# Kernel tuning notes

Hardware: AMD Instinct MI355X
Metric: run time of the kernel (lower is better)

Reference implementation:

```python
import jax, jax.numpy as jnp
import numpy as np

L, B, T, D, H, M = 2, 4, 1024, 256, 4, 1024
EPS = 1e-5  # hk.LayerNorm default


def setup_inputs() -> dict:
    key = jax.random.key(0)
    ks = jax.random.split(key, 12)
    s_in = (2.0 / D) ** 0.5       # VarianceScaling(2.0), fan_in = D
    s_o = (2.0 / (H * D)) ** 0.5  # fan_in = H*D for final projection
    s_m = (1.0 / M) ** 0.5
    g = lambda k, shape, s: jax.random.normal(k, shape, jnp.float32) * s
    return {
        "queries": g(ks[0], (B, T, D), 1.0),
        "Wq": g(ks[1], (L, D, H * D), s_in),
        "bq": jnp.zeros((L, H * D), jnp.float32),
        "Wk": g(ks[2], (L, D, H * D), s_in),
        "bk": jnp.zeros((L, H * D), jnp.float32),
        "Wv": g(ks[3], (L, D, H * D), s_in),
        "bv": jnp.zeros((L, H * D), jnp.float32),
        "Wo": g(ks[4], (L, H * D, D), s_o),
        "bo": jnp.zeros((L, D), jnp.float32),
        "ln1_s": jnp.ones((L, D), jnp.float32),
        "ln1_b": jnp.zeros((L, D), jnp.float32),
        "W1": g(ks[5], (L, D, M), s_in),
        "b1": jnp.zeros((L, M), jnp.float32),
        "W2": g(ks[6], (L, M, D), s_m),
        "b2": jnp.zeros((L, D), jnp.float32),
        "ln2_s": jnp.ones((L, D), jnp.float32),
        "ln2_b": jnp.zeros((L, D), jnp.float32),
    }


def _layernorm(x, s, o):
    m = jnp.mean(x, axis=-1, keepdims=True)
    v = jnp.var(x, axis=-1, keepdims=True)
    return (x - m) * jax.lax.rsqrt(v + EPS) * s + o


def _block(x, Wq, bq, Wk, bk, Wv, bv, Wo, bo, ln1_s, ln1_b, W1, b1, W2, b2, ln2_s, ln2_b):
    # Multi-head self-attention with per-head dim = D (key_size == qkv_size)
    q = (x @ Wq + bq).reshape(B, T, H, D)
    k = (x @ Wk + bk).reshape(B, T, H, D)
    v = (x @ Wv + bv).reshape(B, T, H, D)
    q = q / jnp.sqrt(jnp.float32(D))
    attn = jnp.einsum('bqhd,bkhd->bhqk', q, k)   # [B,H,T,T]
    attn = jax.nn.softmax(attn, axis=-1)
    o = jnp.einsum('bhqk,bkhd->bqhd', attn, v).reshape(B, T, H * D)
    o = o @ Wo + bo
    # post-norm residual 1
    x = _layernorm(o + x, ln1_s, ln1_b)
    # MLP: Linear(D->M) + ReLU + Linear(M->D)
    h = jax.nn.relu(x @ W1 + b1)
    m = h @ W2 + b2
    return _layernorm(m + x, ln2_s, ln2_b)


def reference(queries, Wq, bq, Wk, bk, Wv, bv, Wo, bo, ln1_s, ln1_b,
              W1, b1, W2, b2, ln2_s, ln2_b):
    x = queries
    for i in range(L):
        x = _block(x, Wq[i], bq[i], Wk[i], bk[i], Wv[i], bv[i], Wo[i], bo[i],
                   ln1_s[i], ln1_b[i], W1[i], b1[i], W2[i], b2[i],
                   ln2_s[i], ln2_b[i])
    return x
```

## Files before the change

kernel.cpp:

```cpp
#include <hip/hip_runtime.h>
#include <hip/hip_bf16.h>

#define CL 2
#define CB 4
#define CT 1024
#define CD 256
#define CH 4
#define CM 1024
#define CHD (CH * CD)
#define NROW (CB * CT)

typedef unsigned short ushort_t;
typedef __attribute__((ext_vector_type(8))) short short8v;
typedef __attribute__((ext_vector_type(4))) float float4v;
typedef __attribute__((ext_vector_type(16))) float float16v;

#define LOG2E 1.44269504088896f

__device__ __forceinline__ float bf2f(unsigned short u) {
    return __uint_as_float(((unsigned int)u) << 16);
}
__device__ __forceinline__ unsigned short f2bf(float f) {
    unsigned int x = __float_as_uint(f);
    return (unsigned short)((x + 0x7fffu + ((x >> 16) & 1u)) >> 16);
}

__global__ __launch_bounds__(256) void detect_kernel(
    const ushort_t* __restrict__ w, int n, int* __restrict__ flag)
{
    __shared__ int red[256];
    int c = 0;
    for (int i = threadIdx.x; i < n; i += 256) {
        float v = bf2f(w[i]);
        if (!(fabsf(v) <= 1e6f)) c++;
    }
    red[threadIdx.x] = c;
    __syncthreads();
    for (int s = 128; s > 0; s >>= 1) {
        if (threadIdx.x < s) red[threadIdx.x] += red[threadIdx.x + s];
        __syncthreads();
    }
    if (threadIdx.x == 0) flag[0] = (red[0] < 8) ? 1 : 0;
}

__global__ __launch_bounds__(256) void tconv_all(
    const void* __restrict__ Wq, const void* __restrict__ Wk,
    const void* __restrict__ Wv, const void* __restrict__ W1,
    ushort_t* __restrict__ wqkvT, ushort_t* __restrict__ w1T,
    const int* __restrict__ flagp)
{
    const int fbf = *flagp;
    const int z = blockIdx.z;
    const int which = z >> 1, l = z & 1;
    const void* in = (which == 0) ? Wq : (which == 1) ? Wk
                   : (which == 2) ? Wv : W1;
    ushort_t* out = (which < 3)
        ? wqkvT + (long)l * 3072 * 256 + (long)which * 1024 * 256
        : w1T + (long)l * 1024 * 256;
    const long zi = (long)l * 262144;

    __shared__ float tile[32][33];
    const int r0 = blockIdx.y * 32;
    const int c0 = blockIdx.x * 32;
    const int tx = threadIdx.x & 31;
    const int ty = threadIdx.x >> 5;
#pragma unroll
    for (int i = 0; i < 32; i += 8) {
        const long idx = zi + (long)(r0 + ty + i) * 1024 + c0 + tx;
        tile[ty + i][tx] = fbf ? bf2f(((const ushort_t*)in)[idx])
                               : ((const float*)in)[idx];
    }
    __syncthreads();
#pragma unroll
    for (int i = 0; i < 32; i += 8)
        out[(long)(c0 + ty + i) * 256 + r0 + tx] = f2bf(tile[tx][ty + i]);
}

__global__ __launch_bounds__(256) void qkv_tconv(
    const ushort_t* __restrict__ A, const ushort_t* __restrict__ B,
    const void* __restrict__ bq, const void* __restrict__ bk,
    const void* __restrict__ bv, ushort_t* __restrict__ qk,
    ushort_t* __restrict__ vT,
    const void* __restrict__ Wo, const void* __restrict__ W2,
    ushort_t* __restrict__ wscr,
    long boff, long ioff, const int* __restrict__ flagp)
{
    __shared__ __align__(16) ushort_t As[128 * 40];
    __shared__ __align__(16) ushort_t Bs[128 * 40];
    __shared__ float tile[32][33];

    const int fbf = *flagp;
    const int bx = blockIdx.x;
    const int tid = threadIdx.x;

    if (bx >= 768) {
        const int t = bx - 768;
        const int zx = t & 7;
        const int zy = (t >> 3) & 31;
        const int zz = t >> 8;
        const void* in = zz ? W2 : Wo;
        ushort_t* out = wscr + (long)zz * 262144;
        const int r0 = zy * 32;
        const int c0 = zx * 32;
        const int tx = tid & 31;
        const int ty = tid >> 5;
#pragma unroll
        for (int i = 0; i < 32; i += 8) {
            const long idx = ioff + (long)(r0 + ty + i) * 256 + c0 + tx;
            tile[ty + i][tx] = fbf ? bf2f(((const ushort_t*)in)[idx])
                                   : ((const float*)in)[idx];
        }
        __syncthreads();
#pragma unroll
        for (int i = 0; i < 32; i += 8)
            out[(long)(c0 + ty + i) * 1024 + r0 + tx] = f2bf(tile[tx][ty + i]);
        return;
    }

    const int nt = bx % 24;
    const int mt = bx / 24;
    const long m0 = (long)mt * 128;
    const long n0 = (long)nt * 128;

    const int wave = tid >> 6;
    const int lane = tid & 63;
    const int quad = lane >> 4;
    const int lrow = lane & 15;
    const int wm = (wave >> 1) * 64;
    const int wn = (wave & 1) * 64;

    float4v acc[4][4];
#pragma unroll
    for (int i = 0; i < 4; ++i)
#pragma unroll
        for (int j = 0; j < 4; ++j)
            acc[i][j] = (float4v){0.f, 0.f, 0.f, 0.f};

    for (int k0 = 0; k0 < 256; k0 += 32) {
        __syncthreads();
#pragma unroll
        for (int p = 0; p < 2; ++p) {
            const int c = p * 256 + tid;
            const int row = c >> 2;
            const int kk = (c & 3) << 3;
            *reinterpret_cast<short8v*>(&As[row * 40 + kk]) =
                *reinterpret_cast<const short8v*>(&A[(m0 + row) * 256 + k0 + kk]);
            *reinterpret_cast<short8v*>(&Bs[row * 40 + kk]) =
                *reinterpret_cast<const short8v*>(&B[(n0 + row) * 256 + k0 + kk]);
        }
        __syncthreads();

        short8v af[4], bfv[4];
#pragma unroll
        for (int i = 0; i < 4; ++i) {
            af[i]  = *reinterpret_cast<const short8v*>(&As[(wm + i * 16 + lrow) * 40 + quad * 8]);
            bfv[i] = *reinterpret_cast<const short8v*>(&Bs[(wn + i * 16 + lrow) * 40 + quad * 8]);
        }
#pragma unroll
        for (int mi = 0; mi < 4; ++mi)
#pragma unroll
            for (int ni = 0; ni < 4; ++ni)
                acc[mi][ni] = __builtin_amdgcn_mfma_f32_16x16x32_bf16(
                    af[mi], bfv[ni], acc[mi][ni], 0, 0, 0);
    }

#pragma unroll
    for (int mi = 0; mi < 4; ++mi) {
#pragma unroll
        for (int ni = 0; ni < 4; ++ni) {
            const long col = n0 + wn + ni * 16 + lrow;
            const long row0 = m0 + wm + mi * 16 + quad * 4;
            const void* bp;
            long bn;
            if (col < 1024)      { bp = bq; bn = col; }
            else if (col < 2048) { bp = bk; bn = col - 1024; }
            else                 { bp = bv; bn = col - 2048; }
            const float bias = fbf ? bf2f(((const ushort_t*)bp)[boff + bn])
                                   : ((const float*)bp)[boff + bn];
            if (col < 2048) {
#pragma unroll
                for (int r = 0; r < 4; ++r)
                    qk[(row0 + r) * 2048 + col] = f2bf(acc[mi][ni][r] + bias);
            } else {
                const long d = col - 2048;
                const long addr = ((row0 >> 10) << 2) * 262144 + d * 1024 + (row0 & 1023);
                ushort4 u;
                u.x = f2bf(acc[mi][ni][0] + bias);
                u.y = f2bf(acc[mi][ni][1] + bias);
                u.z = f2bf(acc[mi][ni][2] + bias);
                u.w = f2bf(acc[mi][ni][3] + bias);
                *reinterpret_cast<ushort4*>(&vT[addr]) = u;
            }
        }
    }
}

template <int AMODE>
__global__ __launch_bounds__(256) void mgemm64s(
    const ushort_t* __restrict__ A, const ushort_t* __restrict__ Ap1,
    const float2* __restrict__ ml, const ushort_t* __restrict__ B,
    float* __restrict__ P, int K2, int lda, int ldb)
{
    const int z = blockIdx.z;
    const long m0 = (long)blockIdx.y * 64;
    const long n0 = (long)blockIdx.x * 64;
    const int k_beg = z * K2;

    __shared__ __align__(16) ushort_t As[64 * 72];
    __shared__ __align__(16) ushort_t Bs[64 * 72];

    const int tid = threadIdx.x;
    const int wave = tid >> 6;
    const int lane = tid & 63;
    const int quad = lane >> 4;
    const int lrow = lane & 15;
    const int wm = (wave >> 1) * 32;
    const int wn = (wave & 1) * 32;

    const int ar = tid >> 2;
    const int ak = (tid & 3) << 3;

    float s0h[2] = {0.f, 0.f}, s1h[2] = {0.f, 0.f};
    if constexpr (AMODE == 1) {
        const long m = m0 + ar;
        const int bhbase = ((int)(m >> 10) << 2);
        const int trow = (int)(m & 1023);
        const int h0 = k_beg >> 8;
#pragma unroll
        for (int i = 0; i < 2; ++i) {
            const int bh = bhbase + h0 + i;
            const float2 v0 = ml[bh * 1024 + trow];
            const float2 v1 = ml[(16 + bh) * 1024 + trow];
            const float mm = fmaxf(v0.x, v1.x);
            const float a0 = exp2f(v0.x - mm);
            const float a1 = exp2f(v1.x - mm);
            const float inv = 1.0f / (v0.y * a0 + v1.y * a1);
            s0h[i] = a0 * inv;
            s1h[i] = a1 * inv;
        }
    }

    float4v acc[2][2];
#pragma unroll
    for (int i = 0; i < 2; ++i)
#pragma unroll
        for (int j = 0; j < 2; ++j)
            acc[i][j] = (float4v){0.f, 0.f, 0.f, 0.f};

    for (int k0 = k_beg; k0 < k_beg + K2; k0 += 64) {
        __syncthreads();
#pragma unroll
        for (int p = 0; p < 2; ++p) {
            const int kc = p * 32 + ak;
            if constexpr (AMODE == 0) {
                *reinterpret_cast<short8v*>(&As[ar * 72 + kc]) =
                    *reinterpret_cast<const short8v*>(&A[(m0 + ar) * (long)lda + k0 + kc]);
            } else {
                const long m = m0 + ar;
                const int hi = ((k0 + kc) >> 8) - (k_beg >> 8);
                const float s0 = s0h[hi], s1 = s1h[hi];
                const ushort4 u0a = *reinterpret_cast<const ushort4*>(&A[m * 1024 + k0 + kc]);
                const ushort4 u0b = *reinterpret_cast<const ushort4*>(&A[m * 1024 + k0 + kc + 4]);
                const ushort4 u1a = *reinterpret_cast<const ushort4*>(&Ap1[m * 1024 + k0 + kc]);
                const ushort4 u1b = *reinterpret_cast<const ushort4*>(&Ap1[m * 1024 + k0 + kc + 4]);
                short8v t8;
                t8[0] = (short)f2bf(bf2f(u0a.x) * s0 + bf2f(u1a.x) * s1);
                t8[1] = (short)f2bf(bf2f(u0a.y) * s0 + bf2f(u1a.y) * s1);
                t8[2] = (short)f2bf(bf2f(u0a.z) * s0 + bf2f(u1a.z) * s1);
                t8[3] = (short)f2bf(bf2f(u0a.w) * s0 + bf2f(u1a.w) * s1);
                t8[4] = (short)f2bf(bf2f(u0b.x) * s0 + bf2f(u1b.x) * s1);
                t8[5] = (short)f2bf(bf2f(u0b.y) * s0 + bf2f(u1b.y) * s1);
                t8[6] = (short)f2bf(bf2f(u0b.z) * s0 + bf2f(u1b.z) * s1);
                t8[7] = (short)f2bf(bf2f(u0b.w) * s0 + bf2f(u1b.w) * s1);
                *reinterpret_cast<short8v*>(&As[ar * 72 + kc]) = t8;
            }
            *reinterpret_cast<short8v*>(&Bs[ar * 72 + kc]) =
                *reinterpret_cast<const short8v*>(&B[(n0 + ar) * (long)ldb + k0 + kc]);
        }
        __syncthreads();

#pragma unroll
        for (int kk = 0; kk < 2; ++kk) {
            short8v af[2], bfv[2];
#pragma unroll
            for (int i = 0; i < 2; ++i) {
                af[i]  = *reinterpret_cast<const short8v*>(
                    &As[(wm + i * 16 + lrow) * 72 + kk * 32 + quad * 8]);
                bfv[i] = *reinterpret_cast<const short8v*>(
                    &Bs[(wn + i * 16 + lrow) * 72 + kk * 32 + quad * 8]);
            }
#pragma unroll
            for (int mi = 0; mi < 2; ++mi)
#pragma unroll
                for (int ni = 0; ni < 2; ++ni)
                    acc[mi][ni] = __builtin_amdgcn_mfma_f32_16x16x32_bf16(
                        af[mi], bfv[ni], acc[mi][ni], 0, 0, 0);
        }
    }

    float* Pz = P + (long)z * NROW * CD;
#pragma unroll
    for (int mi = 0; mi < 2; ++mi)
#pragma unroll
        for (int ni = 0; ni < 2; ++ni) {
            const long col = n0 + wn + ni * 16 + lrow;
            const long row0 = m0 + wm + mi * 16 + quad * 4;
#pragma unroll
            for (int r = 0; r < 4; ++r)
                Pz[(row0 + r) * CD + col] = acc[mi][ni][r];
        }
}

template <int RELU>
__global__ __launch_bounds__(256) void mgemm64b(
    const ushort_t* __restrict__ A, const ushort_t* __restrict__ B,
    const void* __restrict__ bias, ushort_t* __restrict__ C,
    int K, int lda, int ldb, int ldc, long boff,
    const int* __restrict__ flagp)
{
    const long m0 = (long)blockIdx.y * 64;
    const long n0 = (long)blockIdx.x * 64;

    __shared__ __align__(16) ushort_t As[64 * 72];
    __shared__ __align__(16) ushort_t Bs[64 * 72];

    const int tid = threadIdx.x;
    const int wave = tid >> 6;
    const int lane = tid & 63;
    const int quad = lane >> 4;
    const int lrow = lane & 15;
    const int wm = (wave >> 1) * 32;
    const int wn = (wave & 1) * 32;

    const int ar = tid >> 2;
    const int ak = (tid & 3) << 3;

    float4v acc[2][2];
#pragma unroll
    for (int i = 0; i < 2; ++i)
#pragma unroll
        for (int j = 0; j < 2; ++j)
            acc[i][j] = (float4v){0.f, 0.f, 0.f, 0.f};

    for (int k0 = 0; k0 < K; k0 += 64) {
        __syncthreads();
#pragma unroll
        for (int p = 0; p < 2; ++p) {
            const int kc = p * 32 + ak;
            *reinterpret_cast<short8v*>(&As[ar * 72 + kc]) =
                *reinterpret_cast<const short8v*>(&A[(m0 + ar) * (long)lda + k0 + kc]);
            *reinterpret_cast<short8v*>(&Bs[ar * 72 + kc]) =
                *reinterpret_cast<const short8v*>(&B[(n0 + ar) * (long)ldb + k0 + kc]);
        }
        __syncthreads();

#pragma unroll
        for (int kk = 0; kk < 2; ++kk) {
            short8v af[2], bfv[2];
#pragma unroll
            for (int i = 0; i < 2; ++i) {
                af[i]  = *reinterpret_cast<const short8v*>(
                    &As[(wm + i * 16 + lrow) * 72 + kk * 32 + quad * 8]);
                bfv[i] = *reinterpret_cast<const short8v*>(
                    &Bs[(wn + i * 16 + lrow) * 72 + kk * 32 + quad * 8]);
            }
#pragma unroll
            for (int mi = 0; mi < 2; ++mi)
#pragma unroll
                for (int ni = 0; ni < 2; ++ni)
                    acc[mi][ni] = __builtin_amdgcn_mfma_f32_16x16x32_bf16(
                        af[mi], bfv[ni], acc[mi][ni], 0, 0, 0);
        }
    }

    const int fbf = *flagp;
#pragma unroll
    for (int mi = 0; mi < 2; ++mi)
#pragma unroll
        for (int ni = 0; ni < 2; ++ni) {
            const long col = n0 + wn + ni * 16 + lrow;
            const long row0 = m0 + wm + mi * 16 + quad * 4;
            const float bv = fbf ? bf2f(((const ushort_t*)bias)[boff + col])
                                 : ((const float*)bias)[boff + col];
#pragma unroll
            for (int r = 0; r < 4; ++r) {
                float v = acc[mi][ni][r] + bv;
                if (RELU) v = fmaxf(v, 0.f);
                C[(row0 + r) * (long)ldc + col] = f2bf(v);
            }
        }
}

__global__ __launch_bounds__(256, 1) void flash_attn(
    const ushort_t* __restrict__ qk, const ushort_t* __restrict__ vT,
    ushort_t* __restrict__ op0, ushort_t* __restrict__ op1,
    float2* __restrict__ ml)
{
    const int bx = blockIdx.x;
    const int bh = bx & 15;
    const int qg = (bx >> 4) & 7;
    const int ck = bx >> 7;
    const int bb = bh >> 2, h = bh & 3;

    __shared__ __align__(16) ushort_t Ks[2][32 * 256];
    __shared__ __align__(16) ushort_t Vs[2][256 * 40];

    const int tid = threadIdx.x;
    const int wave = tid >> 6;
    const int lane = tid & 63;
    const int col = lane & 31;
    const int hi = lane >> 5;
    const int hi8 = hi << 3;

    const long qrow0w = (long)bb * CT + qg * 128 + wave * 32;
    const int qcol = h * 256;
    const int kcol = 1024 + h * 256;
    const long vbase = (long)bh * 256 * 1024;
    const float SC = 0.0625f * LOG2E;
    const int t_beg = ck * 512;

    const int kr_ = tid >> 5;
    const int kc_ = (tid & 31) << 3;
    const int vr_ = tid >> 2;
    const int vc_ = (tid & 3) << 3;

    short8v kreg[4], vreg[4];
#pragma unroll
    for (int i = 0; i < 4; ++i) {
        kreg[i] = *reinterpret_cast<const short8v*>(
            &qk[((long)bb * CT + t_beg + i * 8 + kr_) * 2048 + kcol + kc_]);
        vreg[i] = *reinterpret_cast<const short8v*>(
            &vT[vbase + (long)(i * 64 + vr_) * 1024 + t_beg + vc_]);
    }

    short8v qf[16];
#pragma unroll
    for (int s = 0; s < 16; ++s)
        qf[s] = *reinterpret_cast<const short8v*>(
            &qk[(qrow0w + col) * 2048 + qcol + s * 16 + hi8]);

    float mrun = -1e30f, lrun = 0.f;
    float16v oacc[8];
#pragma unroll
    for (int i = 0; i < 8; ++i)
#pragma unroll
        for (int j = 0; j < 16; ++j) oacc[i][j] = 0.f;

#pragma unroll
    for (int i = 0; i < 4; ++i) {
        const int kr = i * 8 + kr_;
        *reinterpret_cast<short8v*>(
            &Ks[0][kr * 256 + (((tid & 31) ^ kr) << 3)]) = kreg[i];
        *reinterpret_cast<short8v*>(
            &Vs[0][(i * 64 + vr_) * 40 + vc_]) = vreg[i];
    }
    __syncthreads();

    const int krowbase = col * 256;
    const int kxor = col << 4;

    for (int it = 0; it < 16; ++it) {
        const int cur = it & 1;

        if (it < 15) {
            const int tn = t_beg + (it + 1) * 32;
#pragma unroll
            for (int i = 0; i < 4; ++i) {
                kreg[i] = *reinterpret_cast<const short8v*>(
                    &qk[((long)bb * CT + tn + i * 8 + kr_) * 2048 + kcol + kc_]);
                vreg[i] = *reinterpret_cast<const short8v*>(
                    &vT[vbase + (long)(i * 64 + vr_) * 1024 + tn + vc_]);
            }
        }

        float16v sa, sb;
#pragma unroll
        for (int j = 0; j < 16; ++j) { sa[j] = 0.f; sb[j] = 0.f; }
#pragma unroll
        for (int s = 0; s < 16; s += 2) {
            const int o0 = ((s * 32 + hi * 16) ^ kxor) >> 1;
            const int o1 = (((s + 1) * 32 + hi * 16) ^ kxor) >> 1;
            const short8v k0 = *reinterpret_cast<const short8v*>(&Ks[cur][krowbase + o0]);
            const short8v k1 = *reinterpret_cast<const short8v*>(&Ks[cur][krowbase + o1]);
            sa = __builtin_amdgcn_mfma_f32_32x32x16_bf16(k0, qf[s], sa, 0, 0, 0);
            sb = __builtin_amdgcn_mfma_f32_32x32x16_bf16(k1, qf[s + 1], sb, 0, 0, 0);
        }

        float sv[16];
#pragma unroll
        for (int j = 0; j < 16; ++j) sv[j] = (sa[j] + sb[j]) * SC;

        float mx = sv[0];
#pragma unroll
        for (int j = 1; j < 16; ++j) mx = fmaxf(mx, sv[j]);
        mx = fmaxf(mx, __shfl_xor(mx, 32));

        if (__ballot(mx > mrun + 1.0f) != 0ull) {
            const float mnew = fmaxf(mrun, mx);
            const float alpha = exp2f(mrun - mnew);
            mrun = mnew;
            lrun *= alpha;
            float ar[16];
#pragma unroll
            for (int r = 0; r < 16; ++r)
                ar[r] = __shfl(alpha, (r & 3) + 8 * (r >> 2) + (hi << 2));
#pragma unroll
            for (int dt = 0; dt < 8; ++dt)
#pragma unroll
                for (int r = 0; r < 16; ++r)
                    oacc[dt][r] *= ar[r];
        }

        float p[16];
        float s = 0.f;
#pragma unroll
        for (int j = 0; j < 16; ++j) { p[j] = exp2f(sv[j] - mrun); s += p[j]; }
        s += __shfl_xor(s, 32);
        lrun += s;

        const unsigned c01 = (unsigned)f2bf(p[0])  | ((unsigned)f2bf(p[1])  << 16);
        const unsigned c23 = (unsigned)f2bf(p[2])  | ((unsigned)f2bf(p[3])  << 16);
        const unsigned c45 = (unsigned)f2bf(p[4])  | ((unsigned)f2bf(p[5])  << 16);
        const unsigned c67 = (unsigned)f2bf(p[6])  | ((unsigned)f2bf(p[7])  << 16);
        const unsigned d01 = (unsigned)f2bf(p[8])  | ((unsigned)f2bf(p[9])  << 16);
        const unsigned d23 = (unsigned)f2bf(p[10]) | ((unsigned)f2bf(p[11]) << 16);
        const unsigned d45 = (unsigned)f2bf(p[12]) | ((unsigned)f2bf(p[13]) << 16);
        const unsigned d67 = (unsigned)f2bf(p[14]) | ((unsigned)f2bf(p[15]) << 16);
        const unsigned x01 = __shfl_xor(c01, 32);
        const unsigned x23 = __shfl_xor(c23, 32);
        const unsigned x45 = __shfl_xor(c45, 32);
        const unsigned x67 = __shfl_xor(c67, 32);
        const unsigned y01 = __shfl_xor(d01, 32);
        const unsigned y23 = __shfl_xor(d23, 32);
        const unsigned y45 = __shfl_xor(d45, 32);
        const unsigned y67 = __shfl_xor(d67, 32);
        union { unsigned u[4]; short8v v; } pf0, pf1;
        pf0.u[0] = hi ? x45 : c01;
        pf0.u[1] = hi ? x67 : c23;
        pf0.u[2] = hi ? c45 : x01;
        pf0.u[3] = hi ? c67 : x23;
        pf1.u[0] = hi ? y45 : d01;
        pf1.u[1] = hi ? y67 : d23;
        pf1.u[2] = hi ? d45 : y01;
        pf1.u[3] = hi ? d67 : y23;

#pragma unroll
        for (int dt = 0; dt < 8; ++dt) {
            const int vb = (dt * 32 + col) * 40 + hi8;
            const short8v v0 = *reinterpret_cast<const short8v*>(&Vs[cur][vb]);
            const short8v v1 = *reinterpret_cast<const short8v*>(&Vs[cur][vb + 16]);
            oacc[dt] = __builtin_amdgcn_mfma_f32_32x32x16_bf16(pf0.v, v0, oacc[dt], 0, 0, 0);
            oacc[dt] = __builtin_amdgcn_mfma_f32_32x32x16_bf16(pf1.v, v1, oacc[dt], 0, 0, 0);
        }

        if (it < 15) {
            const int nb = cur ^ 1;
#pragma unroll
            for (int i = 0; i < 4; ++i) {
                const int kr = i * 8 + kr_;
                *reinterpret_cast<short8v*>(
                    &Ks[nb][kr * 256 + (((tid & 31) ^ kr) << 3)]) = kreg[i];
                *reinterpret_cast<short8v*>(
                    &Vs[nb][(i * 64 + vr_) * 40 + vc_]) = vreg[i];
            }
            __syncthreads();
        }
    }

    if (lane < 32) {
        const int trow = (int)((qrow0w + lane) & 1023);
        ml[((ck << 4) + bh) * 1024 + trow] = make_float2(mrun, lrun);
    }
    ushort_t* op = ck ? op1 : op0;
#pragma unroll
    for (int dt = 0; dt < 8; ++dt)
#pragma unroll
        for (int r = 0; r < 16; ++r) {
            const int row = (r & 3) + 8 * (r >> 2) + (hi << 2);
            op[(qrow0w + row) * 1024 + (h << 8) + dt * 32 + col] = f2bf(oacc[dt][r]);
        }
}

template <int FINAL>
__global__ __launch_bounds__(256) void ln_p(
    const float* __restrict__ p, const void* __restrict__ gb, long gboff,
    const ushort_t* __restrict__ res, const void* __restrict__ sc,
    const void* __restrict__ bi, void* __restrict__ out, long loff,
    const int* __restrict__ flagp)
{
    const int fbf = *flagp;
    const long row = (long)blockIdx.x * CD;
    const int t = threadIdx.x;
    const float gbv = fbf ? bf2f(((const ushort_t*)gb)[gboff + t])
                          : ((const float*)gb)[gboff + t];
    const float x = p[row + t] + p[(long)NROW * CD + row + t] + gbv + bf2f(res[row + t]);

    __shared__ float r1[256];
    __shared__ float r2[256];
    r1[t] = x;
    r2[t] = x * x;
    __syncthreads();
    for (int s = 128; s > 0; s >>= 1) {
        if (t < s) { r1[t] += r1[t + s]; r2[t] += r2[t + s]; }
        __syncthreads();
    }
    const float mean = r1[0] * (1.0f / CD);
    const float var = r2[0] * (1.0f / CD) - mean * mean;
    const float rstd = rsqrtf(var + 1e-5f);
    const float s_v = fbf ? bf2f(((const ushort_t*)sc)[loff + t]) : ((const float*)sc)[loff + t];
    const float b_v = fbf ? bf2f(((const ushort_t*)bi)[loff + t]) : ((const float*)bi)[loff + t];
    const float y = (x - mean) * rstd * s_v + b_v;
    if constexpr (FINAL) {
        if (fbf) ((ushort_t*)out)[row + t] = f2bf(y);
        else     ((float*)out)[row + t] = y;
    } else {
        ((ushort_t*)out)[row + t] = f2bf(y);
    }
}

__global__ __launch_bounds__(256) void in_convert(
    const void* __restrict__ in, ushort_t* __restrict__ x,
    const int* __restrict__ flagp)
{
    const int fbf = *flagp;
    const long i = ((long)blockIdx.x * 256 + threadIdx.x) << 2;
    if (fbf) {
        *reinterpret_cast<ushort4*>(x + i) =
            *reinterpret_cast<const ushort4*>((const ushort_t*)in + i);
    } else {
        float4 f = *reinterpret_cast<const float4*>((const float*)in + i);
        ushort4 u;
        u.x = f2bf(f.x); u.y = f2bf(f.y); u.z = f2bf(f.z); u.w = f2bf(f.w);
        *reinterpret_cast<ushort4*>(x + i) = u;
    }
}

extern "C" void kernel_launch(void* const* d_in, const int* in_sizes, int n_in,
                              void* d_out, int out_size, void* d_ws, size_t ws_size,
                              hipStream_t stream)
{
    const void* queries = d_in[0];
    const void* Wq = d_in[1];  const void* bq = d_in[2];
    const void* Wk = d_in[3];  const void* bk = d_in[4];
    const void* Wv = d_in[5];  const void* bv = d_in[6];
    const void* Wo = d_in[7];  const void* bo = d_in[8];
    const void* ln1s = d_in[9];  const void* ln1b = d_in[10];
    const void* W1 = d_in[11]; const void* b1 = d_in[12];
    const void* W2 = d_in[13]; const void* b2 = d_in[14];
    const void* ln2s = d_in[15]; const void* ln2b = d_in[16];

    char* p = (char*)d_ws;
    int* flagp = (int*)p;             p += 256;
    ushort_t* wqkvT = (ushort_t*)p;   p += (long)CL * 3072 * 256 * 2;
    ushort_t* w1T   = (ushort_t*)p;   p += (long)CL * 1024 * 256 * 2;
    ushort_t* wscr  = (ushort_t*)p;   p += (long)2 * 256 * 1024 * 2;
    ushort_t* xa    = (ushort_t*)p;   p += (long)NROW * CD * 2;
    ushort_t* qk    = (ushort_t*)p;   p += (long)NROW * 2048 * 2;
    ushort_t* vT    = (ushort_t*)p;   p += (long)16 * 256 * 1024 * 2;
    ushort_t* op0   = (ushort_t*)p;   p += (long)NROW * 1024 * 2;
    ushort_t* op1   = (ushort_t*)p;   p += (long)NROW * 1024 * 2;
    float2*   ml    = (float2*)p;     p += (long)2 * 16 * 1024 * 8;
    ushort_t* h     = vT;
    float*    pgem  = (float*)qk;

    detect_kernel<<<1, 256, 0, stream>>>((const ushort_t*)Wq, 2048, flagp);
    tconv_all<<<dim3(32, 8, 8), 256, 0, stream>>>(
        Wq, Wk, Wv, W1, wqkvT, w1T, flagp);
    in_convert<<<(NROW * CD) / 1024, 256, 0, stream>>>(queries, xa, flagp);

    for (int l = 0; l < CL; ++l) {
        qkv_tconv<<<dim3(1280, 1, 1), 256, 0, stream>>>(
            xa, wqkvT + (long)l * 3072 * 256, bq, bk, bv, qk, vT,
            Wo, W2, wscr, (long)l * 1024, (long)l * 1024 * 256, flagp);
        flash_attn<<<256, 256, 0, stream>>>(qk, vT, op0, op1, ml);
        mgemm64s<1><<<dim3(4, 64, 2), 256, 0, stream>>>(
            op0, op1, ml, wscr, pgem, 512, 1024, 1024);
        ln_p<0><<<NROW, 256, 0, stream>>>(pgem, bo, (long)l * 256, xa,
                                          ln1s, ln1b, xa, (long)l * 256, flagp);
        mgemm64b<1><<<dim3(16, 64, 1), 256, 0, stream>>>(
            xa, w1T + (long)l * 1024 * 256, b1, h,
            256, 256, 256, 1024, (long)l * 1024, flagp);
        mgemm64s<0><<<dim3(4, 64, 2), 256, 0, stream>>>(
            h, nullptr, nullptr, wscr + 262144, pgem, 512, 1024, 1024);
        if (l == CL - 1)
            ln_p<1><<<NROW, 256, 0, stream>>>(pgem, b2, (long)l * 256, xa,
                                              ln2s, ln2b, d_out, (long)l * 256, flagp);
        else
            ln_p<0><<<NROW, 256, 0, stream>>>(pgem, b2, (long)l * 256, xa,
                                              ln2s, ln2b, xa, (long)l * 256, flagp);
    }
}
```

Before: 316.5 us.

## Split flash-attention KV range across two wave groups and merge in LDS

Flash attention blocks now use 512 threads. Two groups of four waves each process half of the block's 512-key chunk, with separate double-buffered K/V shared-memory regions, and their partial softmax states and outputs are merged through LDS at the end. This doubles the waves per block to hide latency and shortens each wave's serial loop. It also raises the rescale threshold from 1 to 8, so online-softmax rescales happen less often, and adds s_setprio around the MFMA sections. The costs are larger shared memory (144KB), a final merge pass, a possible register-pressure change under the new launch bounds, and relying on fp32 headroom for larger unrescaled exponents.

```diff
diff --git a/kernel.cpp b/kernel.cpp
--- a/kernel.cpp
+++ b/kernel.cpp
@@ -391,7 +391,7 @@
         }
 }
 
-__global__ __launch_bounds__(256, 1) void flash_attn(
+__global__ __launch_bounds__(512, 2) void flash_attn(
     const ushort_t* __restrict__ qk, const ushort_t* __restrict__ vT,
     ushort_t* __restrict__ op0, ushort_t* __restrict__ op1,
     float2* __restrict__ ml)
@@ -402,8 +402,7 @@
     const int ck = bx >> 7;
     const int bb = bh >> 2, h = bh & 3;
 
-    __shared__ __align__(16) ushort_t Ks[2][32 * 256];
-    __shared__ __align__(16) ushort_t Vs[2][256 * 40];
+    __shared__ __align__(16) ushort_t smem[73728];
 
     const int tid = threadIdx.x;
     const int wave = tid >> 6;
@@ -412,25 +411,32 @@
     const int hi = lane >> 5;
     const int hi8 = hi << 3;
 
-    const long qrow0w = (long)bb * CT + qg * 128 + wave * 32;
+    const int qsub = wave & 3;
+    const int hf = wave >> 2;
+
+    const long qrow0w = (long)bb * CT + qg * 128 + qsub * 32;
     const int qcol = h * 256;
     const int kcol = 1024 + h * 256;
     const long vbase = (long)bh * 256 * 1024;
     const float SC = 0.0625f * LOG2E;
-    const int t_beg = ck * 512;
-
-    const int kr_ = tid >> 5;
-    const int kc_ = (tid & 31) << 3;
-    const int vr_ = tid >> 2;
-    const int vc_ = (tid & 3) << 3;
+
+    const int sh = tid >> 8;
+    const int st = tid & 255;
+    const int kr_ = st >> 5;
+    const int kc_ = (st & 31) << 3;
+    const int vr_ = st >> 2;
+    const int vc_ = (st & 3) << 3;
+    const int t0s = ck * 512 + sh * 256;
+    ushort_t* KsS = smem + sh * 8192;
+    ushort_t* VsS = smem + 32768 + sh * 10240;
 
     short8v kreg[4], vreg[4];
 #pragma unroll
     for (int i = 0; i < 4; ++i) {
         kreg[i] = *reinterpret_cast<const short8v*>(
-            &qk[((long)bb * CT + t_beg + i * 8 + kr_) * 2048 + kcol + kc_]);
+            &qk[((long)bb * CT + t0s + i * 8 + kr_) * 2048 + kcol + kc_]);
         vreg[i] = *reinterpret_cast<const short8v*>(
-            &vT[vbase + (long)(i * 64 + vr_) * 1024 + t_beg + vc_]);
+            &vT[vbase + (long)(i * 64 + vr_) * 1024 + t0s + vc_]);
     }
 
     short8v qf[16];
@@ -449,21 +455,21 @@
 #pragma unroll
     for (int i = 0; i < 4; ++i) {
         const int kr = i * 8 + kr_;
-        *reinterpret_cast<short8v*>(
-            &Ks[0][kr * 256 + (((tid & 31) ^ kr) << 3)]) = kreg[i];
-        *reinterpret_cast<short8v*>(
-            &Vs[0][(i * 64 + vr_) * 40 + vc_]) = vreg[i];
+        *reinterpret_cast<short8v*>(&KsS[kr * 256 + (((st & 31) ^ kr) << 3)]) = kreg[i];
+        *reinterpret_cast<short8v*>(&VsS[(i * 64 + vr_) * 40 + vc_]) = vreg[i];
     }
     __syncthreads();
 
+    ushort_t* KsW = smem + hf * 8192;
+    ushort_t* VsW = smem + 32768 + hf * 10240;
     const int krowbase = col * 256;
     const int kxor = col << 4;
 
-    for (int it = 0; it < 16; ++it) {
+    for (int it = 0; it < 8; ++it) {
         const int cur = it & 1;
 
-        if (it < 15) {
-            const int tn = t_beg + (it + 1) * 32;
+        if (it < 7) {
+            const int tn = t0s + (it + 1) * 32;
 #pragma unroll
             for (int i = 0; i < 4; ++i) {
                 kreg[i] = *reinterpret_cast<const short8v*>(
@@ -473,18 +479,21 @@
             }
         }
 
+        const ushort_t* Kc = KsW + cur * 16384;
         float16v sa, sb;
 #pragma unroll
         for (int j = 0; j < 16; ++j) { sa[j] = 0.f; sb[j] = 0.f; }
+        __builtin_amdgcn_s_setprio(1);
 #pragma unroll
         for (int s = 0; s < 16; s += 2) {
             const int o0 = ((s * 32 + hi * 16) ^ kxor) >> 1;
             const int o1 = (((s + 1) * 32 + hi * 16) ^ kxor) >> 1;
-            const short8v k0 = *reinterpret_cast<const short8v*>(&Ks[cur][krowbase + o0]);
-            const short8v k1 = *reinterpret_cast<const short8v*>(&Ks[cur][krowbase + o1]);
+            const short8v k0 = *reinterpret_cast<const short8v*>(&Kc[krowbase + o0]);
+            const short8v k1 = *reinterpret_cast<const short8v*>(&Kc[krowbase + o1]);
             sa = __builtin_amdgcn_mfma_f32_32x32x16_bf16(k0, qf[s], sa, 0, 0, 0);
             sb = __builtin_amdgcn_mfma_f32_32x32x16_bf16(k1, qf[s + 1], sb, 0, 0, 0);
         }
+        __builtin_amdgcn_s_setprio(0);
 
         float sv[16];
 #pragma unroll
@@ -495,7 +504,7 @@
         for (int j = 1; j < 16; ++j) mx = fmaxf(mx, sv[j]);
         mx = fmaxf(mx, __shfl_xor(mx, 32));
 
-        if (__ballot(mx > mrun + 1.0f) != 0ull) {
+        if (__ballot(mx > mrun + 8.0f) != 0ull) {
             const float mnew = fmaxf(mrun, mx);
             const float alpha = exp2f(mrun - mnew);
             mrun = mnew;
@@ -544,41 +553,75 @@
         pf1.u[2] = hi ? d45 : y01;
         pf1.u[3] = hi ? d67 : y23;
 
+        const ushort_t* Vc = VsW + cur * 20480;
+        __builtin_amdgcn_s_setprio(1);
 #pragma unroll
         for (int dt = 0; dt < 8; ++dt) {
             const int vb = (dt * 32 + col) * 40 + hi8;
-            const short8v v0 = *reinterpret_cast<const short8v*>(&Vs[cur][vb]);
-            const short8v v1 = *reinterpret_cast<const short8v*>(&Vs[cur][vb + 16]);
+            const short8v v0 = *reinterpret_cast<const short8v*>(&Vc[vb]);
+            const short8v v1 = *reinterpret_cast<const short8v*>(&Vc[vb + 16]);
             oacc[dt] = __builtin_amdgcn_mfma_f32_32x32x16_bf16(pf0.v, v0, oacc[dt], 0, 0, 0);
             oacc[dt] = __builtin_amdgcn_mfma_f32_32x32x16_bf16(pf1.v, v1, oacc[dt], 0, 0, 0);
         }
-
-        if (it < 15) {
+        __builtin_amdgcn_s_setprio(0);
+
+        if (it < 7) {
             const int nb = cur ^ 1;
 #pragma unroll
             for (int i = 0; i < 4; ++i) {
                 const int kr = i * 8 + kr_;
                 *reinterpret_cast<short8v*>(
-                    &Ks[nb][kr * 256 + (((tid & 31) ^ kr) << 3)]) = kreg[i];
+                    &KsS[nb * 16384 + kr * 256 + (((st & 31) ^ kr) << 3)]) = kreg[i];
                 *reinterpret_cast<short8v*>(
-                    &Vs[nb][(i * 64 + vr_) * 40 + vc_]) = vreg[i];
+                    &VsS[nb * 20480 + (i * 64 + vr_) * 40 + vc_]) = vreg[i];
             }
             __syncthreads();
         }
     }
 
-    if (lane < 32) {
-        const int trow = (int)((qrow0w + lane) & 1023);
-        ml[((ck << 4) + bh) * 1024 + trow] = make_float2(mrun, lrun);
-    }
-    ushort_t* op = ck ? op1 : op0;
-#pragma unroll
-    for (int dt = 0; dt < 8; ++dt)
+    __syncthreads();
+    float* xO = (float*)smem;
+    float2* xml = (float2*)((char*)smem + 131072);
+
+    if (hf == 1) {
+#pragma unroll
+        for (int dt = 0; dt < 8; ++dt)
+#pragma unroll
+            for (int r = 0; r < 16; ++r)
+                xO[qsub * 8192 + (dt * 16 + r) * 64 + (hi << 5) + col] = oacc[dt][r];
+        if (hi == 0)
+            xml[qsub * 32 + col] = make_float2(mrun, lrun);
+    }
+    __syncthreads();
+
+    if (hf == 0) {
+        const float2 o2 = xml[qsub * 32 + col];
+        const float mstar = fmaxf(mrun, o2.x);
+        const float a0 = exp2f(mrun - mstar);
+        const float a2 = exp2f(o2.x - mstar);
+        const float lnew = lrun * a0 + o2.y * a2;
+        float ar0[16], ar2[16];
 #pragma unroll
         for (int r = 0; r < 16; ++r) {
-            const int row = (r & 3) + 8 * (r >> 2) + (hi << 2);
-            op[(qrow0w + row) * 1024 + (h << 8) + dt * 32 + col] = f2bf(oacc[dt][r]);
-        }
+            const int li = (r & 3) + 8 * (r >> 2) + (hi << 2);
+            ar0[r] = __shfl(a0, li);
+            ar2[r] = __shfl(a2, li);
+        }
+        if (lane < 32) {
+            const int trow = (int)((qrow0w + lane) & 1023);
+            ml[((ck << 4) + bh) * 1024 + trow] = make_float2(mstar, lnew);
+        }
+        ushort_t* op = ck ? op1 : op0;
+#pragma unroll
+        for (int dt = 0; dt < 8; ++dt)
+#pragma unroll
+            for (int r = 0; r < 16; ++r) {
+                const int row = (r & 3) + 8 * (r >> 2) + (hi << 2);
+                const float of = oacc[dt][r] * ar0[r]
+                    + xO[qsub * 8192 + (dt * 16 + r) * 64 + (hi << 5) + col] * ar2[r];
+                op[(qrow0w + row) * 1024 + (h << 8) + dt * 32 + col] = f2bf(of);
+            }
+    }
 }
 
 template <int FINAL>
@@ -672,7 +715,7 @@
         qkv_tconv<<<dim3(1280, 1, 1), 256, 0, stream>>>(
             xa, wqkvT + (long)l * 3072 * 256, bq, bk, bv, qk, vT,
             Wo, W2, wscr, (long)l * 1024, (long)l * 1024 * 256, flagp);
-        flash_attn<<<256, 256, 0, stream>>>(qk, vT, op0, op1, ml);
+        flash_attn<<<256, 512, 0, stream>>>(qk, vT, op0, op1, ml);
         mgemm64s<1><<<dim3(4, 64, 2), 256, 0, stream>>>(
             op0, op1, ml, wscr, pgem, 512, 1024, 1024);
         ln_p<0><<<NROW, 256, 0, stream>>>(pgem, bo, (long)l * 256, xa,
```

Result: slower. 366.6 us (+15.8%).

## Split attention keys into four chunks and merge partials in output GEMM

Applied to the files above, without the earlier changes.

With a large enough workspace, attention is split into four 256-key chunks instead of two 512-key chunks, which doubles the grid to 512 blocks for better CU occupancy. The Wo GEMM gains a mode that merges four partial outputs using the per-chunk max and sum statistics. A fallback path adds a new 16x16 MFMA flash kernel, also launched with 512 blocks, for small workspaces. Both attention kernels raise wave priority with s_setprio around the MFMA loops. The trade-off is more partial-output traffic and extra merge work in the GEMM A-load path.

```diff
diff --git a/kernel.cpp b/kernel.cpp
--- a/kernel.cpp
+++ b/kernel.cpp
@@ -205,6 +205,7 @@
     const long m0 = (long)blockIdx.y * 64;
     const long n0 = (long)blockIdx.x * 64;
     const int k_beg = z * K2;
+    const long OPSZ = (long)NROW * 1024;
 
     __shared__ __align__(16) ushort_t As[64 * 72];
     __shared__ __align__(16) ushort_t Bs[64 * 72];
@@ -239,6 +240,31 @@
             s1h[i] = a1 * inv;
         }
     }
+    float sh2[2][4];
+    if constexpr (AMODE == 2) {
+        const long m = m0 + ar;
+        const int bhbase = ((int)(m >> 10) << 2);
+        const int trow = (int)(m & 1023);
+        const int h0 = k_beg >> 8;
+#pragma unroll
+        for (int i = 0; i < 2; ++i) {
+            const int bh = bhbase + h0 + i;
+            float mv[4], lv[4];
+#pragma unroll
+            for (int k = 0; k < 4; ++k) {
+                const float2 v = ml[((k << 4) + bh) * 1024 + trow];
+                mv[k] = v.x; lv[k] = v.y;
+            }
+            const float mm = fmaxf(fmaxf(mv[0], mv[1]), fmaxf(mv[2], mv[3]));
+            float den = 0.f;
+            float a[4];
+#pragma unroll
+            for (int k = 0; k < 4; ++k) { a[k] = exp2f(mv[k] - mm); den += lv[k] * a[k]; }
+            const float inv = 1.0f / den;
+#pragma unroll
+            for (int k = 0; k < 4; ++k) sh2[i][k] = a[k] * inv;
+        }
+    }
 
     float4v acc[2][2];
 #pragma unroll
@@ -255,10 +281,10 @@
             if constexpr (AMODE == 0) {
                 *reinterpret_cast<short8v*>(&As[ar * 72 + kc]) =
                     *reinterpret_cast<const short8v*>(&A[(m0 + ar) * (long)lda + k0 + kc]);
-            } else {
+            } else if constexpr (AMODE == 1) {
                 const long m = m0 + ar;
-                const int hi = ((k0 + kc) >> 8) - (k_beg >> 8);
-                const float s0 = s0h[hi], s1 = s1h[hi];
+                const int hh = ((k0 + kc) >> 8) - (k_beg >> 8);
+                const float s0 = s0h[hh], s1 = s1h[hh];
                 const ushort4 u0a = *reinterpret_cast<const ushort4*>(&A[m * 1024 + k0 + kc]);
                 const ushort4 u0b = *reinterpret_cast<const ushort4*>(&A[m * 1024 + k0 + kc + 4]);
                 const ushort4 u1a = *reinterpret_cast<const ushort4*>(&Ap1[m * 1024 + k0 + kc]);
@@ -273,6 +299,29 @@
                 t8[6] = (short)f2bf(bf2f(u0b.z) * s0 + bf2f(u1b.z) * s1);
                 t8[7] = (short)f2bf(bf2f(u0b.w) * s0 + bf2f(u1b.w) * s1);
                 *reinterpret_cast<short8v*>(&As[ar * 72 + kc]) = t8;
+            } else {
+                const long m = m0 + ar;
+                const int hh = ((k0 + kc) >> 8) - (k_beg >> 8);
+                float e0 = 0.f, e1 = 0.f, e2 = 0.f, e3 = 0.f;
+                float e4 = 0.f, e5 = 0.f, e6 = 0.f, e7 = 0.f;
+#pragma unroll
+                for (int k = 0; k < 4; ++k) {
+                    const float s = sh2[hh][k];
+                    const ushort4 ua = *reinterpret_cast<const ushort4*>(
+                        &A[k * OPSZ + m * 1024 + k0 + kc]);
+                    const ushort4 ub = *reinterpret_cast<const ushort4*>(
+                        &A[k * OPSZ + m * 1024 + k0 + kc + 4]);
+                    e0 += bf2f(ua.x) * s; e1 += bf2f(ua.y) * s;
+                    e2 += bf2f(ua.z) * s; e3 += bf2f(ua.w) * s;
+                    e4 += bf2f(ub.x) * s; e5 += bf2f(ub.y) * s;
+                    e6 += bf2f(ub.z) * s; e7 += bf2f(ub.w) * s;
+                }
+                short8v t8;
+                t8[0] = (short)f2bf(e0); t8[1] = (short)f2bf(e1);
+                t8[2] = (short)f2bf(e2); t8[3] = (short)f2bf(e3);
+                t8[4] = (short)f2bf(e4); t8[5] = (short)f2bf(e5);
+                t8[6] = (short)f2bf(e6); t8[7] = (short)f2bf(e7);
+                *reinterpret_cast<short8v*>(&As[ar * 72 + kc]) = t8;
             }
             *reinterpret_cast<short8v*>(&Bs[ar * 72 + kc]) =
                 *reinterpret_cast<const short8v*>(&B[(n0 + ar) * (long)ldb + k0 + kc]);
@@ -391,13 +440,178 @@
         }
 }
 
-__global__ __launch_bounds__(256, 1) void flash_attn(
+__global__ __launch_bounds__(256) void flash_attn2(
     const ushort_t* __restrict__ qk, const ushort_t* __restrict__ vT,
     ushort_t* __restrict__ op0, ushort_t* __restrict__ op1,
     float2* __restrict__ ml)
 {
     const int bx = blockIdx.x;
     const int bh = bx & 15;
+    const int qt = (bx >> 4) & 15;
+    const int ck = bx >> 8;
+    const int b = bh >> 2, h = bh & 3;
+
+    __shared__ __align__(16) ushort_t Ks[2][32 * 264];
+    __shared__ __align__(16) ushort_t Vs[2][256 * 40];
+    __shared__ __align__(16) ushort_t Ps[4][16 * 40];
+
+    const int tid = threadIdx.x;
+    const int wave = tid >> 6;
+    const int lane = tid & 63;
+    const int quad = lane >> 4;
+    const int lrow = lane & 15;
+
+    const long qrow0 = (long)b * CT + qt * 64;
+    const int qcol = h * 256;
+    const int kcol = 1024 + h * 256;
+    const long vbase = (long)bh * 256 * 1024;
+    const float SC = 0.0625f * LOG2E;
+
+    short8v qf[8];
+#pragma unroll
+    for (int kk = 0; kk < 8; ++kk)
+        qf[kk] = *reinterpret_cast<const short8v*>(
+            &qk[(qrow0 + wave * 16 + lrow) * 2048 + qcol + kk * 32 + quad * 8]);
+
+    float mrun = -1e30f, lrun = 0.f;
+    float4v oacc[16];
+#pragma unroll
+    for (int i = 0; i < 16; ++i) oacc[i] = (float4v){0.f, 0.f, 0.f, 0.f};
+
+    const int krow_b = tid >> 5;
+    const int kcol8  = (tid & 31) * 8;
+    const int vrow_b = tid >> 2;
+    const int vcol8  = (tid & 3) * 8;
+
+    short8v kreg[4], vreg[4];
+
+    const int t_beg = ck * 512;
+
+#pragma unroll
+    for (int p = 0; p < 4; ++p) {
+        kreg[p] = *reinterpret_cast<const short8v*>(
+            &qk[((long)b * CT + t_beg + p * 8 + krow_b) * 2048 + kcol + kcol8]);
+        vreg[p] = *reinterpret_cast<const short8v*>(
+            &vT[vbase + (long)(p * 64 + vrow_b) * 1024 + t_beg + vcol8]);
+    }
+
+    for (int t0 = t_beg; t0 < t_beg + 512; t0 += 32) {
+        const int bsel = (t0 >> 5) & 1;
+
+#pragma unroll
+        for (int p = 0; p < 4; ++p) {
+            *reinterpret_cast<short8v*>(&Ks[bsel][(p * 8 + krow_b) * 264 + kcol8]) = kreg[p];
+            *reinterpret_cast<short8v*>(&Vs[bsel][(p * 64 + vrow_b) * 40 + vcol8]) = vreg[p];
+        }
+
+        if (t0 + 32 < t_beg + 512) {
+            const int tn = t0 + 32;
+#pragma unroll
+            for (int p = 0; p < 4; ++p) {
+                kreg[p] = *reinterpret_cast<const short8v*>(
+                    &qk[((long)b * CT + tn + p * 8 + krow_b) * 2048 + kcol + kcol8]);
+                vreg[p] = *reinterpret_cast<const short8v*>(
+                    &vT[vbase + (long)(p * 64 + vrow_b) * 1024 + tn + vcol8]);
+            }
+        }
+
+        __syncthreads();
+
+        float4v sacc[2];
+        sacc[0] = (float4v){0.f, 0.f, 0.f, 0.f};
+        sacc[1] = (float4v){0.f, 0.f, 0.f, 0.f};
+        __builtin_amdgcn_s_setprio(1);
+#pragma unroll
+        for (int kk = 0; kk < 8; ++kk) {
+#pragma unroll
+            for (int ni = 0; ni < 2; ++ni) {
+                short8v bk = *reinterpret_cast<const short8v*>(
+                    &Ks[bsel][(ni * 16 + lrow) * 264 + kk * 32 + quad * 8]);
+                sacc[ni] = __builtin_amdgcn_mfma_f32_16x16x32_bf16(
+                    bk, qf[kk], sacc[ni], 0, 0, 0);
+            }
+        }
+        __builtin_amdgcn_s_setprio(0);
+#pragma unroll
+        for (int ni = 0; ni < 2; ++ni)
+#pragma unroll
+            for (int r = 0; r < 4; ++r)
+                sacc[ni][r] *= SC;
+
+        float mx = fmaxf(fmaxf(fmaxf(sacc[0][0], sacc[0][1]),
+                               fmaxf(sacc[0][2], sacc[0][3])),
+                         fmaxf(fmaxf(sacc[1][0], sacc[1][1]),
+                               fmaxf(sacc[1][2], sacc[1][3])));
+        mx = fmaxf(mx, __shfl_xor(mx, 16));
+        mx = fmaxf(mx, __shfl_xor(mx, 32));
+
+        if (__ballot(mx > mrun + 1.0f) != 0ull) {
+            const float mnew = fmaxf(mrun, mx);
+            const float alpha = exp2f(mrun - mnew);
+            mrun = mnew;
+            lrun *= alpha;
+            float a4[4];
+#pragma unroll
+            for (int r = 0; r < 4; ++r)
+                a4[r] = __shfl(alpha, quad * 4 + r);
+#pragma unroll
+            for (int ni = 0; ni < 16; ++ni)
+#pragma unroll
+                for (int r = 0; r < 4; ++r)
+                    oacc[ni][r] *= a4[r];
+        }
+
+        float s = 0.f;
+#pragma unroll
+        for (int ni = 0; ni < 2; ++ni) {
+            ushort4 pu;
+#pragma unroll
+            for (int r = 0; r < 4; ++r) {
+                const float pv = exp2f(sacc[ni][r] - mrun);
+                s += pv;
+                (&pu.x)[r] = f2bf(pv);
+            }
+            *reinterpret_cast<ushort4*>(
+                &Ps[wave][lrow * 40 + ni * 16 + quad * 4]) = pu;
+        }
+        s += __shfl_xor(s, 16);
+        s += __shfl_xor(s, 32);
+        lrun += s;
+
+        {
+            short8v ap = *reinterpret_cast<const short8v*>(
+                &Ps[wave][lrow * 40 + quad * 8]);
+            __builtin_amdgcn_s_setprio(1);
+#pragma unroll
+            for (int ni = 0; ni < 16; ++ni) {
+                short8v bv = *reinterpret_cast<const short8v*>(
+                    &Vs[bsel][(ni * 16 + lrow) * 40 + quad * 8]);
+                oacc[ni] = __builtin_amdgcn_mfma_f32_16x16x32_bf16(
+                    ap, bv, oacc[ni], 0, 0, 0);
+            }
+            __builtin_amdgcn_s_setprio(0);
+        }
+    }
+
+    if (quad == 0)
+        ml[((ck << 4) + bh) * 1024 + qt * 64 + wave * 16 + lrow] =
+            make_float2(mrun, lrun);
+
+    ushort_t* op = ck ? op1 : op0;
+#pragma unroll
+    for (int ni = 0; ni < 16; ++ni)
+#pragma unroll
+        for (int r = 0; r < 4; ++r)
+            op[(qrow0 + wave * 16 + quad * 4 + r) * 1024 + (h << 8) + ni * 16 + lrow]
+                = f2bf(oacc[ni][r]);
+}
+
+__global__ __launch_bounds__(256, 1) void flash_attn4(
+    const ushort_t* __restrict__ qk, const ushort_t* __restrict__ vT,
+    ushort_t* __restrict__ opb, float2* __restrict__ ml)
+{
+    const int bx = blockIdx.x;
+    const int bh = bx & 15;
     const int qg = (bx >> 4) & 7;
     const int ck = bx >> 7;
     const int bb = bh >> 2, h = bh & 3;
@@ -417,7 +631,7 @@
     const int kcol = 1024 + h * 256;
     const long vbase = (long)bh * 256 * 1024;
     const float SC = 0.0625f * LOG2E;
-    const int t_beg = ck * 512;
+    const int t_beg = ck * 256;
 
     const int kr_ = tid >> 5;
     const int kc_ = (tid & 31) << 3;
@@ -459,10 +673,10 @@
     const int krowbase = col * 256;
     const int kxor = col << 4;
 
-    for (int it = 0; it < 16; ++it) {
+    for (int it = 0; it < 8; ++it) {
         const int cur = it & 1;
 
-        if (it < 15) {
+        if (it < 7) {
             const int tn = t_beg + (it + 1) * 32;
 #pragma unroll
             for (int i = 0; i < 4; ++i) {
@@ -476,6 +690,7 @@
         float16v sa, sb;
 #pragma unroll
         for (int j = 0; j < 16; ++j) { sa[j] = 0.f; sb[j] = 0.f; }
+        __builtin_amdgcn_s_setprio(1);
 #pragma unroll
         for (int s = 0; s < 16; s += 2) {
             const int o0 = ((s * 32 + hi * 16) ^ kxor) >> 1;
@@ -485,6 +700,7 @@
             sa = __builtin_amdgcn_mfma_f32_32x32x16_bf16(k0, qf[s], sa, 0, 0, 0);
             sb = __builtin_amdgcn_mfma_f32_32x32x16_bf16(k1, qf[s + 1], sb, 0, 0, 0);
         }
+        __builtin_amdgcn_s_setprio(0);
 
         float sv[16];
 #pragma unroll
@@ -544,6 +760,7 @@
         pf1.u[2] = hi ? d45 : y01;
         pf1.u[3] = hi ? d67 : y23;
 
+        __builtin_amdgcn_s_setprio(1);
 #pragma unroll
         for (int dt = 0; dt < 8; ++dt) {
             const int vb = (dt * 32 + col) * 40 + hi8;
@@ -552,8 +769,9 @@
             oacc[dt] = __builtin_amdgcn_mfma_f32_32x32x16_bf16(pf0.v, v0, oacc[dt], 0, 0, 0);
             oacc[dt] = __builtin_amdgcn_mfma_f32_32x32x16_bf16(pf1.v, v1, oacc[dt], 0, 0, 0);
         }
-
-        if (it < 15) {
+        __builtin_amdgcn_s_setprio(0);
+
+        if (it < 7) {
             const int nb = cur ^ 1;
 #pragma unroll
             for (int i = 0; i < 4; ++i) {
@@ -571,7 +789,7 @@
         const int trow = (int)((qrow0w + lane) & 1023);
         ml[((ck << 4) + bh) * 1024 + trow] = make_float2(mrun, lrun);
     }
-    ushort_t* op = ck ? op1 : op0;
+    ushort_t* op = opb + (long)ck * ((long)NROW * 1024);
 #pragma unroll
     for (int dt = 0; dt < 8; ++dt)
 #pragma unroll
@@ -649,6 +867,8 @@
     const void* W2 = d_in[13]; const void* b2 = d_in[14];
     const void* ln2s = d_in[15]; const void* ln2b = d_in[16];
 
+    const bool big = ws_size >= 67108864ULL;
+
     char* p = (char*)d_ws;
     int* flagp = (int*)p;             p += 256;
     ushort_t* wqkvT = (ushort_t*)p;   p += (long)CL * 3072 * 256 * 2;
@@ -657,9 +877,14 @@
     ushort_t* xa    = (ushort_t*)p;   p += (long)NROW * CD * 2;
     ushort_t* qk    = (ushort_t*)p;   p += (long)NROW * 2048 * 2;
     ushort_t* vT    = (ushort_t*)p;   p += (long)16 * 256 * 1024 * 2;
-    ushort_t* op0   = (ushort_t*)p;   p += (long)NROW * 1024 * 2;
-    ushort_t* op1   = (ushort_t*)p;   p += (long)NROW * 1024 * 2;
-    float2*   ml    = (float2*)p;     p += (long)2 * 16 * 1024 * 8;
+    ushort_t* opb   = (ushort_t*)p;
+    if (big) p += (long)4 * NROW * 1024 * 2;
+    else     p += (long)2 * NROW * 1024 * 2;
+    float2*   ml    = (float2*)p;
+    if (big) p += (long)4 * 16 * 1024 * 8;
+    else     p += (long)2 * 16 * 1024 * 8;
+    ushort_t* op0   = opb;
+    ushort_t* op1   = opb + (long)NROW * 1024;
     ushort_t* h     = vT;
     float*    pgem  = (float*)qk;
 
@@ -672,9 +897,15 @@
         qkv_tconv<<<dim3(1280, 1, 1), 256, 0, stream>>>(
             xa, wqkvT + (long)l * 3072 * 256, bq, bk, bv, qk, vT,
             Wo, W2, wscr, (long)l * 1024, (long)l * 1024 * 256, flagp);
-        flash_attn<<<256, 256, 0, stream>>>(qk, vT, op0, op1, ml);
-        mgemm64s<1><<<dim3(4, 64, 2), 256, 0, stream>>>(
-            op0, op1, ml, wscr, pgem, 512, 1024, 1024);
+        if (big) {
+            flash_attn4<<<512, 256, 0, stream>>>(qk, vT, opb, ml);
+            mgemm64s<2><<<dim3(4, 64, 2), 256, 0, stream>>>(
+                opb, nullptr, ml, wscr, pgem, 512, 1024, 1024);
+        } else {
+            flash_attn2<<<512, 256, 0, stream>>>(qk, vT, op0, op1, ml);
+            mgemm64s<1><<<dim3(4, 64, 2), 256, 0, stream>>>(
+                op0, op1, ml, wscr, pgem, 512, 1024, 1024);
+        }
         ln_p<0><<<NROW, 256, 0, stream>>>(pgem, bo, (long)l * 256, xa,
                                           ln1s, ln1b, xa, (long)l * 256, flagp);
         mgemm64b<1><<<dim3(16, 64, 1), 256, 0, stream>>>(
```

Result: slower. 344.8 us (+9.0%).
